# Kernel tuning notes

Hardware: AMD Instinct MI355X
Metric: run time of the kernel (lower is better)

The kernel has to match this reference:

```python
import jax, jax.numpy as jnp
import numpy as np

B, N = 2048, 110
H1, F1 = 5, 24   # gat1: 5 heads, 24-dim, concat
H2, F2 = 3, 3    # gat2: 3 heads, 3-dim, average
NEG = -9e15
ALPHA = 0.2  # tf.nn.leaky_relu default alpha


def _glorot(key, shape):
    fan_in, fan_out = shape[-2], shape[-1]
    lim = np.sqrt(6.0 / (fan_in + fan_out))
    return jax.random.uniform(key, shape, jnp.float32, -lim, lim)


def setup_inputs() -> dict:
    key = jax.random.key(0)
    ks = jax.random.split(key, 12)
    X = jax.random.normal(ks[0], (B, N, N), jnp.float32)
    # sparse-ish 0/1 adjacency with self-loops
    A = (jax.random.uniform(ks[1], (B, N, N)) < 0.3).astype(jnp.float32)
    A = jnp.maximum(A, jnp.eye(N, dtype=jnp.float32)[None])
    return {
        "X": X,
        "A": A,
        "M": jax.random.normal(ks[2], (N, N), jnp.float32),  # learnable mask
        "W1": _glorot(ks[3], (H1, N, F1)),
        "as1": _glorot(ks[4], (H1, F1, 1))[..., 0],
        "an1": _glorot(ks[5], (H1, F1, 1))[..., 0],
        "b1": jnp.zeros((F1,), jnp.float32),
        "W2": _glorot(ks[6], (H2, H1 * F1, F2)),
        "as2": _glorot(ks[7], (H2, F2, 1))[..., 0],
        "an2": _glorot(ks[8], (H2, F2, 1))[..., 0],
        "b2": jnp.zeros((F2,), jnp.float32),
        "fc1_w": _glorot(ks[9], (F2, 1)),
        "fc2_w": _glorot(ks[10], (N, N)),
    }


def _gat_layer(X, A, W, a_s, a_n, b, concat):
    # X: [B,N,Din]; W: [H,Din,F]; a_s,a_n: [H,F]; b: [F]
    feats = jnp.einsum('bni,hif->bhnf', X, W)               # per-head projection
    e_s = jnp.einsum('bhnf,hf->bhn', feats, a_s)
    e_n = jnp.einsum('bhnf,hf->bhn', feats, a_n)
    e = jax.nn.leaky_relu(e_s[..., :, None] + e_n[..., None, :], ALPHA)  # [B,H,N,N]
    e = jnp.where(A[:, None] > 0.0, e, NEG)                  # adjacency mask
    attn = jax.nn.softmax(e, axis=-1)
    h = jnp.einsum('bhnm,bhmf->bhnf', attn, feats) + b       # aggregate + bias
    if concat:
        h = jax.nn.leaky_relu(h, ALPHA)
        b_, hh, n_, f_ = h.shape
        return h.transpose(0, 2, 1, 3).reshape(b_, n_, hh * f_)
    # 'average': add heads / H, then activation
    return jax.nn.leaky_relu(h.mean(axis=1), ALPHA)


def reference(X, A, M, W1, as1, an1, b1, W2, as2, an2, b2, fc1_w, fc2_w):
    Xm = X * jax.nn.sigmoid(M)[None]                         # learnable mask gating
    h1 = _gat_layer(Xm, A, W1, as1, an1, b1, concat=True)    # [B,N,H1*F1]
    h2 = _gat_layer(h1, A, W2, as2, an2, b2, concat=False)   # [B,N,F2]
    node_prob = jax.nn.sigmoid(h2 @ fc1_w)                   # [B,N,1]
    t = node_prob.reshape(-1, N)                             # [B,N]
    attn_prob = jax.nn.softmax(t @ fc2_w, axis=-1)           # [B,N]
    return jnp.sum(t * attn_prob, axis=1, keepdims=True)     # [B,1]
```

## Files before the change

### kernel.cpp

```cpp
#include <hip/hip_runtime.h>
#include <math.h>

#define NB 2048
#define NV 110
#define NH1 5
#define NF1 24
#define NH2 3
#define NF2 3
#define C1 (NH1*NF1)
#define LALPHA 0.2f

constexpr int NN = NV*NV;
constexpr int T1 = 512;
constexpr int KP = 136;
constexpr int W1ROWS = 144;

typedef _Float16 f16;
typedef f16  f16x8 __attribute__((ext_vector_type(8)));
typedef f16  f16x4 __attribute__((ext_vector_type(4)));
typedef float f32x4 __attribute__((ext_vector_type(4)));

__device__ __forceinline__ f32x4 mfma16(f16x8 a, f16x8 b, f32x4 c) {
  return __builtin_amdgcn_mfma_f32_16x16x32_f16(a, b, c, 0, 0, 0);
}
__device__ __forceinline__ float lrelu(float x){ return x > 0.f ? x : LALPHA*x; }
__device__ __forceinline__ float frcp(float x){ return __builtin_amdgcn_rcpf(x); }
__device__ __forceinline__ float sigm(float x){ return frcp(1.f+__expf(-x)); }
__device__ __forceinline__ float expm4(float v){
  return __builtin_amdgcn_exp2f(fmaf(v, 1.442695041f, -5.770780163f));
}
__device__ __forceinline__ float wmax(float v){
  #pragma unroll
  for (int d=32; d; d>>=1) v = fmaxf(v, __shfl_xor(v,d));
  return v;
}
__device__ __forceinline__ float wsum(float v){
  #pragma unroll
  for (int d=32; d; d>>=1) v += __shfl_xor(v,d);
  return v;
}
__device__ __forceinline__ f32x4 ld4u(const float* p){
  f32x4 v; __builtin_memcpy(&v, p, 16); return v;
}

__global__ void precomp_kernel(const float* __restrict__ M, const float* __restrict__ W1,
                               const float* __restrict__ as1, const float* __restrict__ an1,
                               const float* __restrict__ W2, const float* __restrict__ as2,
                               const float* __restrict__ an2, const float* __restrict__ fc2w,
                               float* __restrict__ Msig, f16* __restrict__ W1tg,
                               f16* __restrict__ W2tg, f16* __restrict__ fc2tg) {
  const int i = blockIdx.x*256 + threadIdx.x;
  if (i < NN) {
    Msig[i] = sigm(M[i]);
  } else if (i < NN + W1ROWS*KP) {
    const int j = i - NN, f = j/KP, k = j%KP;
    float v = 0.f;
    if (k < NV) {
      if (f < C1) {
        v = W1[(f/NF1)*(NV*NF1) + k*NF1 + (f%NF1)];
      } else if (f >= 128 && f < 133) {
        const int h = f - 128;
        for (int ff = 0; ff < NF1; ++ff)
          v += W1[h*(NV*NF1) + k*NF1 + ff] * as1[h*NF1 + ff];
      } else if (f >= 133 && f < 138) {
        const int h = f - 133;
        for (int ff = 0; ff < NF1; ++ff)
          v += W1[h*(NV*NF1) + k*NF1 + ff] * an1[h*NF1 + ff];
      }
    }
    W1tg[f*KP + k] = (f16)v;
  } else if (i < NN + W1ROWS*KP + 16*KP) {
    const int j = i - NN - W1ROWS*KP, r = j/KP, k = j%KP;
    float v = 0.f;
    if (k < C1) {
      if (r < 9) {
        v = W2[(r/NF2)*(C1*NF2) + k*NF2 + (r%NF2)];
      } else if (r < 12) {
        const int g = r - 9;
        for (int f2 = 0; f2 < NF2; ++f2)
          v += W2[g*(C1*NF2) + k*NF2 + f2] * as2[g*NF2 + f2];
      } else if (r < 15) {
        const int g = r - 12;
        for (int f2 = 0; f2 < NF2; ++f2)
          v += W2[g*(C1*NF2) + k*NF2 + f2] * an2[g*NF2 + f2];
      }
    }
    W2tg[r*KP + k] = (f16)v;
  } else if (i < NN + W1ROWS*KP + 16*KP + 112*KP) {
    const int j = i - NN - W1ROWS*KP - 16*KP, col = j/KP, k = j%KP;
    float v = 0.f;
    if (col < NV && k < NV) v = fc2w[k*NV + col];
    fc2tg[col*KP + k] = (f16)v;
  }
}

__global__ __launch_bounds__(T1, 4) void gat_fused(
  const float* __restrict__ X, const float* __restrict__ A,
  const float* __restrict__ Msig, const f16* __restrict__ W1tg,
  const float* __restrict__ b1,  const f16* __restrict__ W2tg,
  const float* __restrict__ b2,  const float* __restrict__ fc1w,
  const f16* __restrict__ fc2tg, float* __restrict__ out)
{
  __shared__ __attribute__((aligned(16))) f16 sXm [112*KP];
  __shared__ __attribute__((aligned(16))) f16 sFt [128*KP];
  __shared__ __attribute__((aligned(16))) f16 sF2t[16*KP];
  __shared__ float sES[NH1*112];
  __shared__ float sEN[NH1*112];
  __shared__ unsigned long long sAM[2*NV];
  __shared__ float sCMB[3][112][4];

  const int b = blockIdx.x, tid = threadIdx.x;
  const int wave = tid >> 6, lane = tid & 63;
  const int lr = lane & 15, lh = lane >> 4;
  const float* __restrict__ Xb = X + (size_t)b*NN;
  const float* __restrict__ Ab = A + (size_t)b*NN;

  float* const sT = sES;
  float* const sS = sES + 112;
  f16*   const t16 = sF2t;

  for (int i = tid; i < (112*KP)/8; i += T1) ((uint4*)sXm )[i] = uint4{0,0,0,0};
  for (int i = tid; i < (128*KP)/8; i += T1) ((uint4*)sFt )[i] = uint4{0,0,0,0};
  for (int i = tid; i < (16*KP)/8;  i += T1) ((uint4*)sF2t)[i] = uint4{0,0,0,0};
  __syncthreads();

  for (int t = tid; t < NV*28; t += T1) {
    const int n = t/28, c = t%28, k = 4*c;
    if (c < 27) {
      f32x4 x = ld4u(Xb + n*NV + k);
      f32x4 m = ld4u(Msig + n*NV + k);
      f16x4 v;
      #pragma unroll
      for (int j = 0; j < 4; ++j) v[j] = (f16)(x[j]*m[j]);
      *(f16x4*)&sXm[n*KP + k] = v;
    } else {
      sXm[n*KP + 108] = (f16)(Xb[n*NV+108]*Msig[n*NV+108]);
      sXm[n*KP + 109] = (f16)(Xb[n*NV+109]*Msig[n*NV+109]);
    }
  }
  #pragma unroll
  for (int i = 0; i < 14; ++i) {
    const int n = wave + 8*i;
    if (n < NV) {
      unsigned long long m0 = __ballot(Ab[n*NV + lane] > 0.f);
      const int mm = 64 + lane;
      unsigned long long m1 = __ballot((mm < NV) && (Ab[n*NV + mm] > 0.f));
      if (lane == 0) { sAM[2*n] = m0; sAM[2*n+1] = m1; }
    }
  }
  f16x8 bW[4], bL[4];
  #pragma unroll
  for (int k = 0; k < 4; ++k)
    bW[k] = *(const f16x8*)&W1tg[(wave*16 + lr)*KP + k*32 + lh*8];
  if (wave < 2) {
    #pragma unroll
    for (int k = 0; k < 4; ++k)
      bL[k] = *(const f16x8*)&W1tg[(128 + lr)*KP + k*32 + lh*8];
  }
  __syncthreads();

  #pragma unroll
  for (int m = 0; m < 7; ++m) {
    f32x4 acc = {0.f,0.f,0.f,0.f};
    #pragma unroll
    for (int k = 0; k < 4; ++k) {
      f16x8 af = *(const f16x8*)&sXm[(m*16 + lr)*KP + k*32 + lh*8];
      acc = mfma16(af, bW[k], acc);
    }
    f16x4 v;
    #pragma unroll
    for (int r = 0; r < 4; ++r) v[r] = (f16)acc[r];
    *(f16x4*)&sFt[(wave*16 + lr)*KP + m*16 + lh*4] = v;
  }
  if (wave < 2) {
    const int mlo = wave ? 4 : 0, mhi = wave ? 7 : 4;
    for (int m = mlo; m < mhi; ++m) {
      f32x4 acc = {0.f,0.f,0.f,0.f};
      #pragma unroll
      for (int k = 0; k < 4; ++k) {
        f16x8 af = *(const f16x8*)&sXm[(m*16 + lr)*KP + k*32 + lh*8];
        acc = mfma16(af, bL[k], acc);
      }
      const int mg0 = m*16 + lh*4;
      if (lr < 5)       *(f32x4*)&sES[lr*112 + mg0] = acc;
      else if (lr < 10) *(f32x4*)&sEN[(lr-5)*112 + mg0] = acc;
    }
  }
  __syncthreads();

  const int half = wave & 1, q = wave >> 1;
  const int nrow = half*64 + lane;
  const int m0base = q*32;
  const int nchunk = (q == 3) ? 2 : 4;

  const int nt = wave & 1, mh = wave >> 1;
  f16 h1r[5][2][4];
  #pragma unroll
  for (int p = 0; p < 5; ++p) {
    if (nrow < NV) {
      const float es = sES[p*112 + nrow];
      const unsigned long long am = sAM[2*nrow + (q>>1)];
      float psum = 0.f;
      for (int c = 0; c < nchunk; ++c) {
        const int m0 = m0base + c*8;
        const f32x4 enA = *(const f32x4*)&sEN[p*112 + m0];
        const f32x4 enB = *(const f32x4*)&sEN[p*112 + m0 + 4];
        const unsigned bits = (unsigned)(am >> (m0 & 63)) & 0xFFu;
        f16x8 pk;
        #pragma unroll
        for (int j = 0; j < 8; ++j) {
          float v = es + ((j < 4) ? enA[j] : enB[j-4]);
          v = fmaxf(v, LALPHA*v);
          v = ((bits >> j) & 1u) ? v : -1e30f;
          const float e = expm4(v);
          psum += e;
          pk[j] = (f16)e;
        }
        *(f16x8*)&sXm[nrow*KP + m0] = pk;
      }
      sCMB[0][nrow][q] = psum;
    }
    __syncthreads();
    f16x8 bf[4];
    #pragma unroll
    for (int k = 0; k < 4; ++k)
      bf[k] = *(const f16x8*)&sFt[(p*NF1 + nt*16 + lr)*KP + k*32 + lh*8];
    const int fl = nt*16 + lr;
    const float bv = (fl < NF1) ? b1[fl] : 0.f;
    #pragma unroll
    for (int mi = 0; mi < 2; ++mi) {
      const int m = 2*mh + mi;
      if (m < 7) {
        f32x4 acc = {0.f,0.f,0.f,0.f};
        #pragma unroll
        for (int k = 0; k < 4; ++k) {
          f16x8 af = *(const f16x8*)&sXm[(m*16 + lr)*KP + k*32 + lh*8];
          acc = mfma16(af, bf[k], acc);
        }
        const int mg0 = m*16 + lh*4;
        #pragma unroll
        for (int r = 0; r < 4; ++r) {
          const f32x4 cm = *(const f32x4*)&sCMB[0][mg0 + r][0];
          const float inv = frcp(cm[0]+cm[1]+cm[2]+cm[3]);
          h1r[p][mi][r] = (f16)lrelu(acc[r]*inv + bv);
        }
      }
    }
    __syncthreads();
  }

  {
    const int fl = nt*16 + lr;
    if (fl < NF1) {
      #pragma unroll
      for (int p = 0; p < 5; ++p) {
        #pragma unroll
        for (int mi = 0; mi < 2; ++mi) {
          const int m = 2*mh + mi;
          if (m < 7) {
            #pragma unroll
            for (int r = 0; r < 4; ++r) {
              const int mg = m*16 + lh*4 + r;
              if (mg < NV) sXm[mg*KP + p*NF1 + fl] = h1r[p][mi][r];
            }
          }
        }
      }
    }
  }
  __syncthreads();

  if (wave < 7) {
    f16x8 bW2[4];
    #pragma unroll
    for (int k = 0; k < 4; ++k)
      bW2[k] = *(const f16x8*)&W2tg[lr*KP + k*32 + lh*8];
    f32x4 acc = {0.f,0.f,0.f,0.f};
    #pragma unroll
    for (int k = 0; k < 4; ++k) {
      f16x8 af = *(const f16x8*)&sXm[(wave*16 + lr)*KP + k*32 + lh*8];
      acc = mfma16(af, bW2[k], acc);
    }
    const int mg0 = wave*16 + lh*4;
    if (lr < 9) {
      #pragma unroll
      for (int r = 0; r < 4; ++r) {
        const int mg = mg0 + r;
        if (mg < NV) sF2t[lr*KP + mg] = (f16)acc[r];
      }
    } else if (lr < 12) {
      *(f32x4*)&sES[(lr-9)*112 + mg0] = acc;
    } else if (lr < 15) {
      *(f32x4*)&sEN[(lr-12)*112 + mg0] = acc;
    }
  }
  __syncthreads();

  auto sweep2 = [&](const float* __restrict__ esr, const float* __restrict__ enr,
                    float* __restrict__ cmb, f16* __restrict__ dst) {
    if (nrow < NV) {
      const float es = esr[nrow];
      const unsigned long long am = sAM[2*nrow + (q>>1)];
      float psum = 0.f;
      for (int c = 0; c < nchunk; ++c) {
        const int m0 = m0base + c*8;
        const f32x4 enA = *(const f32x4*)&enr[m0];
        const f32x4 enB = *(const f32x4*)&enr[m0 + 4];
        const unsigned bits = (unsigned)(am >> (m0 & 63)) & 0xFFu;
        f16x8 pk;
        #pragma unroll
        for (int j = 0; j < 8; ++j) {
          float v = es + ((j < 4) ? enA[j] : enB[j-4]);
          v = fmaxf(v, LALPHA*v);
          v = ((bits >> j) & 1u) ? v : -1e30f;
          const float e = expm4(v);
          psum += e;
          pk[j] = (f16)e;
        }
        *(f16x8*)&dst[nrow*KP + m0] = pk;
      }
      cmb[nrow*4 + q] = psum;
    }
  };
  auto gemm3 = [&](const f16* __restrict__ Pb, int g, f32x4& acc) {
    if (wave < 7) {
      const int brow = (lr < NF2) ? (g*NF2 + lr) : 15;
      f16x8 bf2[4];
      #pragma unroll
      for (int k = 0; k < 4; ++k)
        bf2[k] = *(const f16x8*)&sF2t[brow*KP + k*32 + lh*8];
      #pragma unroll
      for (int k = 0; k < 4; ++k) {
        f16x8 af = *(const f16x8*)&Pb[(wave*16 + lr)*KP + k*32 + lh*8];
        acc = mfma16(af, bf2[k], acc);
      }
    }
  };

  f32x4 acc2_0 = {0.f,0.f,0.f,0.f};
  f32x4 acc2_1 = {0.f,0.f,0.f,0.f};
  f32x4 acc2_2 = {0.f,0.f,0.f,0.f};
  sweep2(&sES[0],   &sEN[0],   &sCMB[0][0][0], sXm);
  __syncthreads();
  gemm3(sXm, 0, acc2_0);
  sweep2(&sES[112], &sEN[112], &sCMB[1][0][0], sFt);
  __syncthreads();
  gemm3(sFt, 1, acc2_1);
  sweep2(&sES[224], &sEN[224], &sCMB[2][0][0], sXm);
  __syncthreads();
  gemm3(sXm, 2, acc2_2);
  __syncthreads();

  if (wave < 7) {
    const int mg0 = wave*16 + lh*4;
    const float fcv = (lr < NF2) ? fc1w[lr] : 0.f;
    const float b2v = (lr < NF2) ? b2[lr]  : 0.f;
    #pragma unroll
    for (int r = 0; r < 4; ++r) {
      const int mg = mg0 + r;
      const f32x4 cm0 = *(const f32x4*)&sCMB[0][mg][0];
      const f32x4 cm1 = *(const f32x4*)&sCMB[1][mg][0];
      const f32x4 cm2 = *(const f32x4*)&sCMB[2][mg][0];
      const float hsum = acc2_0[r]*frcp(cm0[0]+cm0[1]+cm0[2]+cm0[3])
                       + acc2_1[r]*frcp(cm1[0]+cm1[1]+cm1[2]+cm1[3])
                       + acc2_2[r]*frcp(cm2[0]+cm2[1]+cm2[2]+cm2[3]);
      float hv = (lr < NF2) ? lrelu(hsum*(1.f/NH2) + b2v)*fcv : 0.f;
      hv += __shfl_xor(hv, 1);
      hv += __shfl_xor(hv, 2);
      hv += __shfl_xor(hv, 4);
      hv += __shfl_xor(hv, 8);
      if (lr == 0 && mg < NV) sT[mg] = sigm(hv);
    }
  }
  __syncthreads();
  for (int i = tid; i < 16*KP; i += T1) {
    const int k = i % KP;
    t16[i] = (k < NV) ? (f16)sT[k] : (f16)0.f;
  }
  __syncthreads();
  if (wave < 7) {
    f32x4 acc = {0.f,0.f,0.f,0.f};
    #pragma unroll
    for (int k = 0; k < 4; ++k) {
      f16x8 af = *(const f16x8*)&t16[lr*KP + k*32 + lh*8];
      f16x8 bf = *(const f16x8*)&fc2tg[(wave*16 + lr)*KP + k*32 + lh*8];
      acc = mfma16(af, bf, acc);
    }
    const int col = wave*16 + lr;
    if (lh == 0 && col < NV) sS[col] = acc[0];
  }
  __syncthreads();
  if (wave == 0) {
    const float s0 = sS[lane];
    const float s1 = (64+lane < NV) ? sS[64+lane] : -1e38f;
    const float mx = wmax(fmaxf(s0, s1));
    const float p0 = __expf(s0 - mx);
    const float p1 = (64+lane < NV) ? __expf(s1 - mx) : 0.f;
    const float sum = wsum(p0 + p1);
    float val = sT[lane]*p0 + ((64+lane < NV) ? sT[64+lane]*p1 : 0.f);
    val = wsum(val);
    if (lane == 0) out[b] = val*frcp(sum);
  }
}

extern "C" void kernel_launch(void* const* d_in, const int* in_sizes, int n_in,
                              void* d_out, int out_size, void* d_ws, size_t ws_size,
                              hipStream_t stream) {
  const float* X   = (const float*)d_in[0];
  const float* A   = (const float*)d_in[1];
  const float* M   = (const float*)d_in[2];
  const float* W1  = (const float*)d_in[3];
  const float* as1 = (const float*)d_in[4];
  const float* an1 = (const float*)d_in[5];
  const float* b1  = (const float*)d_in[6];
  const float* W2  = (const float*)d_in[7];
  const float* as2 = (const float*)d_in[8];
  const float* an2 = (const float*)d_in[9];
  const float* b2  = (const float*)d_in[10];
  const float* fc1 = (const float*)d_in[11];
  const float* fc2 = (const float*)d_in[12];
  float* out = (float*)d_out;

  float* Msig = (float*)d_ws;
  f16* W1tg  = (f16*)((char*)d_ws + 48400);
  f16* W2tg  = (f16*)((char*)d_ws + 48400 + W1ROWS*KP*2);
  f16* fc2tg = (f16*)((char*)d_ws + 48400 + W1ROWS*KP*2 + 16*KP*2);

  const int pre_items = NN + W1ROWS*KP + 16*KP + 112*KP;
  precomp_kernel<<<(pre_items + 255)/256, 256, 0, stream>>>(
      M, W1, as1, an1, W2, as2, an2, fc2, Msig, W1tg, W2tg, fc2tg);
  gat_fused<<<NB, T1, 0, stream>>>(X, A, Msig, W1tg, b1, W2tg,
                                   b2, fc1, fc2tg, out);
}
```

Baseline: 178.8 us.

## Keep attention probabilities in registers as MFMA operands, dropping LDS round-trip

Each wave now owns 16 output rows. It computes the masked leaky-relu exponentials for its rows directly in the MFMA A-operand register layout, instead of writing them to shared memory and reading them back. Row sums are reduced with cross-lane shuffles, and each layer-2 head is fused with its aggregation GEMM. This removes per-head barriers and LDS traffic, and only the padding regions are zero-initialised rather than whole buffers. The cost is that only 7 of 8 waves do the softmax sweep, and register pressure rises.

```diff
diff --git a/kernel.cpp b/kernel.cpp
--- a/kernel.cpp
+++ b/kernel.cpp
@@ -104,13 +104,16 @@
   __shared__ __attribute__((aligned(16))) f16 sXm [112*KP];
   __shared__ __attribute__((aligned(16))) f16 sFt [128*KP];
   __shared__ __attribute__((aligned(16))) f16 sF2t[16*KP];
-  __shared__ float sES[NH1*112];
-  __shared__ float sEN[NH1*112];
-  __shared__ unsigned long long sAM[2*NV];
-  __shared__ float sCMB[3][112][4];
+  __shared__ __attribute__((aligned(16))) float sES [NH1*112];
+  __shared__ __attribute__((aligned(16))) float sEN [NH1*128];
+  __shared__ __attribute__((aligned(16))) float sES2[NH2*112];
+  __shared__ __attribute__((aligned(16))) float sEN2[NH2*128];
+  __shared__ unsigned long long sAM[2*112];
+  __shared__ __attribute__((aligned(16))) float sROW [112];
+  __shared__ __attribute__((aligned(16))) float sROW2[3*112];
 
   const int b = blockIdx.x, tid = threadIdx.x;
-  const int wave = tid >> 6, lane = tid & 63;
+  const int wv = tid >> 6, lane = tid & 63;
   const int lr = lane & 15, lh = lane >> 4;
   const float* __restrict__ Xb = X + (size_t)b*NN;
   const float* __restrict__ Ab = A + (size_t)b*NN;
@@ -119,10 +122,22 @@
   float* const sS = sES + 112;
   f16*   const t16 = sF2t;
 
-  for (int i = tid; i < (112*KP)/8; i += T1) ((uint4*)sXm )[i] = uint4{0,0,0,0};
-  for (int i = tid; i < (128*KP)/8; i += T1) ((uint4*)sFt )[i] = uint4{0,0,0,0};
-  for (int i = tid; i < (16*KP)/8;  i += T1) ((uint4*)sF2t)[i] = uint4{0,0,0,0};
-  __syncthreads();
+  for (int n = tid; n < 110; n += T1) {
+    *(unsigned*)&sXm[n*KP + 110] = 0u;
+    *(uint4*)&sXm[n*KP + 112] = uint4{0,0,0,0};
+    *(uint4*)&sXm[n*KP + 120] = uint4{0,0,0,0};
+    *(uint4*)&sXm[n*KP + 128] = uint4{0,0,0,0};
+  }
+  for (int i = tid; i < 2*KP/8; i += T1)
+    ((uint4*)&sXm[110*KP])[i] = uint4{0,0,0,0};
+  for (int n = tid; n < 128; n += T1) {
+    *(uint4*)&sFt[n*KP + 112] = uint4{0,0,0,0};
+    *(uint4*)&sFt[n*KP + 120] = uint4{0,0,0,0};
+    *(uint4*)&sFt[n*KP + 128] = uint4{0,0,0,0};
+  }
+  for (int i = tid; i < (16*KP)/8; i += T1)
+    ((uint4*)sF2t)[i] = uint4{0,0,0,0};
+  if (tid < 4) sAM[220 + tid] = 0ull;
 
   for (int t = tid; t < NV*28; t += T1) {
     const int n = t/28, c = t%28, k = 4*c;
@@ -140,7 +155,7 @@
   }
   #pragma unroll
   for (int i = 0; i < 14; ++i) {
-    const int n = wave + 8*i;
+    const int n = wv + 8*i;
     if (n < NV) {
       unsigned long long m0 = __ballot(Ab[n*NV + lane] > 0.f);
       const int mm = 64 + lane;
@@ -151,8 +166,8 @@
   f16x8 bW[4], bL[4];
   #pragma unroll
   for (int k = 0; k < 4; ++k)
-    bW[k] = *(const f16x8*)&W1tg[(wave*16 + lr)*KP + k*32 + lh*8];
-  if (wave < 2) {
+    bW[k] = *(const f16x8*)&W1tg[(wv*16 + lr)*KP + k*32 + lh*8];
+  if (wv < 2) {
     #pragma unroll
     for (int k = 0; k < 4; ++k)
       bL[k] = *(const f16x8*)&W1tg[(128 + lr)*KP + k*32 + lh*8];
@@ -170,10 +185,10 @@
     f16x4 v;
     #pragma unroll
     for (int r = 0; r < 4; ++r) v[r] = (f16)acc[r];
-    *(f16x4*)&sFt[(wave*16 + lr)*KP + m*16 + lh*4] = v;
-  }
-  if (wave < 2) {
-    const int mlo = wave ? 4 : 0, mhi = wave ? 7 : 4;
+    *(f16x4*)&sFt[(wv*16 + lr)*KP + m*16 + lh*4] = v;
+  }
+  if (wv < 2) {
+    const int mlo = wv ? 4 : 0, mhi = wv ? 7 : 4;
     for (int m = mlo; m < mhi; ++m) {
       f32x4 acc = {0.f,0.f,0.f,0.f};
       #pragma unroll
@@ -183,86 +198,76 @@
       }
       const int mg0 = m*16 + lh*4;
       if (lr < 5)       *(f32x4*)&sES[lr*112 + mg0] = acc;
-      else if (lr < 10) *(f32x4*)&sEN[(lr-5)*112 + mg0] = acc;
-    }
-  }
-  __syncthreads();
-
-  const int half = wave & 1, q = wave >> 1;
-  const int nrow = half*64 + lane;
-  const int m0base = q*32;
-  const int nchunk = (q == 3) ? 2 : 4;
-
-  const int nt = wave & 1, mh = wave >> 1;
+      else if (lr < 10) *(f32x4*)&sEN[(lr-5)*128 + mg0] = acc;
+    }
+  }
+  __syncthreads();
+
+  const int row  = wv*16 + lr;
+  const int arow = (row < 112) ? row : 0;
+  const unsigned long long am0 = sAM[2*arow], am1 = sAM[2*arow+1];
+  const float bvt0 = (lr < NF1) ? b1[lr] : 0.f;
+  const float bvt1 = (16 + lr < NF1) ? b1[16 + lr] : 0.f;
+
   f16 h1r[5][2][4];
+  f16x8 pa[4];
   #pragma unroll
   for (int p = 0; p < 5; ++p) {
-    if (nrow < NV) {
-      const float es = sES[p*112 + nrow];
-      const unsigned long long am = sAM[2*nrow + (q>>1)];
+    if (wv < 7) {
+      const float es = sES[p*112 + row];
       float psum = 0.f;
-      for (int c = 0; c < nchunk; ++c) {
-        const int m0 = m0base + c*8;
-        const f32x4 enA = *(const f32x4*)&sEN[p*112 + m0];
-        const f32x4 enB = *(const f32x4*)&sEN[p*112 + m0 + 4];
-        const unsigned bits = (unsigned)(am >> (m0 & 63)) & 0xFFu;
+      #pragma unroll
+      for (int k = 0; k < 4; ++k) {
+        const int cb = k*32 + lh*8;
+        const f32x4 enA = *(const f32x4*)&sEN[p*128 + cb];
+        const f32x4 enB = *(const f32x4*)&sEN[p*128 + cb + 4];
+        const unsigned bits = (unsigned)(((cb & 64) ? am1 : am0) >> (cb & 63)) & 0xFFu;
         f16x8 pk;
         #pragma unroll
         for (int j = 0; j < 8; ++j) {
           float v = es + ((j < 4) ? enA[j] : enB[j-4]);
           v = fmaxf(v, LALPHA*v);
-          v = ((bits >> j) & 1u) ? v : -1e30f;
+          v = (bits & (1u << j)) ? v : -1e30f;
           const float e = expm4(v);
           psum += e;
           pk[j] = (f16)e;
         }
-        *(f16x8*)&sXm[nrow*KP + m0] = pk;
-      }
-      sCMB[0][nrow][q] = psum;
+        pa[k] = pk;
+      }
+      psum += __shfl_xor(psum, 16);
+      psum += __shfl_xor(psum, 32);
+      if (lh == 0) sROW[row] = psum;
     }
     __syncthreads();
-    f16x8 bf[4];
-    #pragma unroll
-    for (int k = 0; k < 4; ++k)
-      bf[k] = *(const f16x8*)&sFt[(p*NF1 + nt*16 + lr)*KP + k*32 + lh*8];
-    const int fl = nt*16 + lr;
-    const float bv = (fl < NF1) ? b1[fl] : 0.f;
-    #pragma unroll
-    for (int mi = 0; mi < 2; ++mi) {
-      const int m = 2*mh + mi;
-      if (m < 7) {
+    if (wv < 7) {
+      #pragma unroll
+      for (int nt2 = 0; nt2 < 2; ++nt2) {
         f32x4 acc = {0.f,0.f,0.f,0.f};
         #pragma unroll
         for (int k = 0; k < 4; ++k) {
-          f16x8 af = *(const f16x8*)&sXm[(m*16 + lr)*KP + k*32 + lh*8];
-          acc = mfma16(af, bf[k], acc);
+          f16x8 bf = *(const f16x8*)&sFt[(p*NF1 + nt2*16 + lr)*KP + k*32 + lh*8];
+          acc = mfma16(pa[k], bf, acc);
         }
-        const int mg0 = m*16 + lh*4;
+        const f32x4 rs = *(const f32x4*)&sROW[wv*16 + lh*4];
+        const float bv = nt2 ? bvt1 : bvt0;
         #pragma unroll
-        for (int r = 0; r < 4; ++r) {
-          const f32x4 cm = *(const f32x4*)&sCMB[0][mg0 + r][0];
-          const float inv = frcp(cm[0]+cm[1]+cm[2]+cm[3]);
-          h1r[p][mi][r] = (f16)lrelu(acc[r]*inv + bv);
-        }
-      }
-    }
-    __syncthreads();
-  }
-
-  {
-    const int fl = nt*16 + lr;
-    if (fl < NF1) {
-      #pragma unroll
-      for (int p = 0; p < 5; ++p) {
-        #pragma unroll
-        for (int mi = 0; mi < 2; ++mi) {
-          const int m = 2*mh + mi;
-          if (m < 7) {
-            #pragma unroll
-            for (int r = 0; r < 4; ++r) {
-              const int mg = m*16 + lh*4 + r;
-              if (mg < NV) sXm[mg*KP + p*NF1 + fl] = h1r[p][mi][r];
-            }
+        for (int r = 0; r < 4; ++r)
+          h1r[p][nt2][r] = (f16)lrelu(acc[r]*frcp(rs[r]) + bv);
+      }
+    }
+  }
+
+  if (wv < 7) {
+    #pragma unroll
+    for (int p = 0; p < 5; ++p) {
+      #pragma unroll
+      for (int nt2 = 0; nt2 < 2; ++nt2) {
+        const int fl = nt2*16 + lr;
+        if (fl < NF1) {
+          #pragma unroll
+          for (int r = 0; r < 4; ++r) {
+            const int mg = wv*16 + lh*4 + r;
+            if (mg < NV) sXm[mg*KP + p*NF1 + fl] = h1r[p][nt2][r];
           }
         }
       }
@@ -270,18 +275,15 @@
   }
   __syncthreads();
 
-  if (wave < 7) {
-    f16x8 bW2[4];
-    #pragma unroll
-    for (int k = 0; k < 4; ++k)
-      bW2[k] = *(const f16x8*)&W2tg[lr*KP + k*32 + lh*8];
+  if (wv < 7) {
     f32x4 acc = {0.f,0.f,0.f,0.f};
     #pragma unroll
     for (int k = 0; k < 4; ++k) {
-      f16x8 af = *(const f16x8*)&sXm[(wave*16 + lr)*KP + k*32 + lh*8];
-      acc = mfma16(af, bW2[k], acc);
-    }
-    const int mg0 = wave*16 + lh*4;
+      f16x8 af = *(const f16x8*)&sXm[(wv*16 + lr)*KP + k*32 + lh*8];
+      f16x8 bf = *(const f16x8*)&W2tg[lr*KP + k*32 + lh*8];
+      acc = mfma16(af, bf, acc);
+    }
+    const int mg0 = wv*16 + lh*4;
     if (lr < 9) {
       #pragma unroll
       for (int r = 0; r < 4; ++r) {
@@ -289,87 +291,74 @@
         if (mg < NV) sF2t[lr*KP + mg] = (f16)acc[r];
       }
     } else if (lr < 12) {
-      *(f32x4*)&sES[(lr-9)*112 + mg0] = acc;
+      *(f32x4*)&sES2[(lr-9)*112 + mg0] = acc;
     } else if (lr < 15) {
-      *(f32x4*)&sEN[(lr-12)*112 + mg0] = acc;
-    }
-  }
-  __syncthreads();
-
-  auto sweep2 = [&](const float* __restrict__ esr, const float* __restrict__ enr,
-                    float* __restrict__ cmb, f16* __restrict__ dst) {
-    if (nrow < NV) {
-      const float es = esr[nrow];
-      const unsigned long long am = sAM[2*nrow + (q>>1)];
+      *(f32x4*)&sEN2[(lr-12)*128 + mg0] = acc;
+    }
+  }
+  __syncthreads();
+
+  f32x4 a2_0 = {0.f,0.f,0.f,0.f};
+  f32x4 a2_1 = {0.f,0.f,0.f,0.f};
+  f32x4 a2_2 = {0.f,0.f,0.f,0.f};
+  if (wv < 7) {
+    #pragma unroll
+    for (int g = 0; g < 3; ++g) {
+      const float es = sES2[g*112 + row];
       float psum = 0.f;
-      for (int c = 0; c < nchunk; ++c) {
-        const int m0 = m0base + c*8;
-        const f32x4 enA = *(const f32x4*)&enr[m0];
-        const f32x4 enB = *(const f32x4*)&enr[m0 + 4];
-        const unsigned bits = (unsigned)(am >> (m0 & 63)) & 0xFFu;
+      #pragma unroll
+      for (int k = 0; k < 4; ++k) {
+        const int cb = k*32 + lh*8;
+        const f32x4 enA = *(const f32x4*)&sEN2[g*128 + cb];
+        const f32x4 enB = *(const f32x4*)&sEN2[g*128 + cb + 4];
+        const unsigned bits = (unsigned)(((cb & 64) ? am1 : am0) >> (cb & 63)) & 0xFFu;
         f16x8 pk;
         #pragma unroll
         for (int j = 0; j < 8; ++j) {
           float v = es + ((j < 4) ? enA[j] : enB[j-4]);
           v = fmaxf(v, LALPHA*v);
-          v = ((bits >> j) & 1u) ? v : -1e30f;
+          v = (bits & (1u << j)) ? v : -1e30f;
           const float e = expm4(v);
           psum += e;
           pk[j] = (f16)e;
         }
-        *(f16x8*)&dst[nrow*KP + m0] = pk;
-      }
-      cmb[nrow*4 + q] = psum;
-    }
-  };
-  auto gemm3 = [&](const f16* __restrict__ Pb, int g, f32x4& acc) {
-    if (wave < 7) {
+        pa[k] = pk;
+      }
+      psum += __shfl_xor(psum, 16);
+      psum += __shfl_xor(psum, 32);
+      if (lh == 0) sROW2[g*112 + row] = psum;
       const int brow = (lr < NF2) ? (g*NF2 + lr) : 15;
-      f16x8 bf2[4];
-      #pragma unroll
-      for (int k = 0; k < 4; ++k)
-        bf2[k] = *(const f16x8*)&sF2t[brow*KP + k*32 + lh*8];
       #pragma unroll
       for (int k = 0; k < 4; ++k) {
-        f16x8 af = *(const f16x8*)&Pb[(wave*16 + lr)*KP + k*32 + lh*8];
-        acc = mfma16(af, bf2[k], acc);
-      }
-    }
-  };
-
-  f32x4 acc2_0 = {0.f,0.f,0.f,0.f};
-  f32x4 acc2_1 = {0.f,0.f,0.f,0.f};
-  f32x4 acc2_2 = {0.f,0.f,0.f,0.f};
-  sweep2(&sES[0],   &sEN[0],   &sCMB[0][0][0], sXm);
-  __syncthreads();
-  gemm3(sXm, 0, acc2_0);
-  sweep2(&sES[112], &sEN[112], &sCMB[1][0][0], sFt);
-  __syncthreads();
-  gemm3(sFt, 1, acc2_1);
-  sweep2(&sES[224], &sEN[224], &sCMB[2][0][0], sXm);
-  __syncthreads();
-  gemm3(sXm, 2, acc2_2);
-  __syncthreads();
-
-  if (wave < 7) {
-    const int mg0 = wave*16 + lh*4;
+        f16x8 bf = *(const f16x8*)&sF2t[brow*KP + k*32 + lh*8];
+        if (g == 0)      a2_0 = mfma16(pa[k], bf, a2_0);
+        else if (g == 1) a2_1 = mfma16(pa[k], bf, a2_1);
+        else             a2_2 = mfma16(pa[k], bf, a2_2);
+      }
+    }
+  }
+  __syncthreads();
+
+  if (wv < 7) {
+    const int mg0 = wv*16 + lh*4;
     const float fcv = (lr < NF2) ? fc1w[lr] : 0.f;
     const float b2v = (lr < NF2) ? b2[lr]  : 0.f;
+    const f32x4 rs0 = *(const f32x4*)&sROW2[0*112 + mg0];
+    const f32x4 rs1 = *(const f32x4*)&sROW2[1*112 + mg0];
+    const f32x4 rs2 = *(const f32x4*)&sROW2[2*112 + mg0];
     #pragma unroll
     for (int r = 0; r < 4; ++r) {
-      const int mg = mg0 + r;
-      const f32x4 cm0 = *(const f32x4*)&sCMB[0][mg][0];
-      const f32x4 cm1 = *(const f32x4*)&sCMB[1][mg][0];
-      const f32x4 cm2 = *(const f32x4*)&sCMB[2][mg][0];
-      const float hsum = acc2_0[r]*frcp(cm0[0]+cm0[1]+cm0[2]+cm0[3])
-                       + acc2_1[r]*frcp(cm1[0]+cm1[1]+cm1[2]+cm1[3])
-                       + acc2_2[r]*frcp(cm2[0]+cm2[1]+cm2[2]+cm2[3]);
+      const float hsum = a2_0[r]*frcp(rs0[r]) + a2_1[r]*frcp(rs1[r])
+                       + a2_2[r]*frcp(rs2[r]);
       float hv = (lr < NF2) ? lrelu(hsum*(1.f/NH2) + b2v)*fcv : 0.f;
       hv += __shfl_xor(hv, 1);
       hv += __shfl_xor(hv, 2);
       hv += __shfl_xor(hv, 4);
       hv += __shfl_xor(hv, 8);
-      if (lr == 0 && mg < NV) sT[mg] = sigm(hv);
+      if (lr == 0) {
+        const int mg = mg0 + r;
+        if (mg < NV) sT[mg] = sigm(hv);
+      }
     }
   }
   __syncthreads();
@@ -378,19 +367,19 @@
     t16[i] = (k < NV) ? (f16)sT[k] : (f16)0.f;
   }
   __syncthreads();
-  if (wave < 7) {
+  if (wv < 7) {
     f32x4 acc = {0.f,0.f,0.f,0.f};
     #pragma unroll
     for (int k = 0; k < 4; ++k) {
       f16x8 af = *(const f16x8*)&t16[lr*KP + k*32 + lh*8];
-      f16x8 bf = *(const f16x8*)&fc2tg[(wave*16 + lr)*KP + k*32 + lh*8];
+      f16x8 bf = *(const f16x8*)&fc2tg[(wv*16 + lr)*KP + k*32 + lh*8];
       acc = mfma16(af, bf, acc);
     }
-    const int col = wave*16 + lr;
+    const int col = wv*16 + lr;
     if (lh == 0 && col < NV) sS[col] = acc[0];
   }
   __syncthreads();
-  if (wave == 0) {
+  if (wv == 0) {
     const float s0 = sS[lane];
     const float s1 = (64+lane < NV) ? sS[64+lane] : -1e38f;
     const float mx = wmax(fmaxf(s0, s1));
```

New measurement: 160.3 us. 1.12x faster.
